# Kernel tuning notes

Measured on AMD Instinct MI355X. Metric: run time of the kernel, lower is better.

The kernel has to match this reference:

```python
import jax, jax.numpy as jnp
import numpy as np
from jax import lax


def _qconv_w(r, i, j, k):
    # Hamilton-product block kernel: components are (out/4, in/4, kh, kw) -> (out, in, kh, kw)
    row_r = jnp.concatenate([r, -i, -j, -k], axis=1)
    row_i = jnp.concatenate([i, r, -k, j], axis=1)
    row_j = jnp.concatenate([j, k, r, -i], axis=1)
    row_k = jnp.concatenate([k, -j, i, r], axis=1)
    return jnp.concatenate([row_r, row_i, row_j, row_k], axis=0)


def _conv3x3(x, W, b):
    y = lax.conv_general_dilated(x, W, window_strides=(1, 1), padding=((1, 1), (1, 1)),
                                 dimension_numbers=('NCHW', 'OIHW', 'NCHW'))
    return y + b[None, :, None, None]


def _qbn(x, gamma, beta, eps=1e-5):
    # Quaternion BN: global per-component mean, shared scalar quaternion variance
    r, i, j, k = jnp.split(x, 4, axis=1)
    dr, di, dj, dk = r - r.mean(), i - i.mean(), j - j.mean(), k - k.mean()
    var = (dr * dr + di * di + dj * dj + dk * dk).mean()
    inv = 1.0 / jnp.sqrt(var + eps)
    br, bi, bj, bk = jnp.split(beta, 4, axis=1)
    return jnp.concatenate([gamma * dr * inv + br, gamma * di * inv + bi,
                            gamma * dj * inv + bj, gamma * dk * inv + bk], axis=1)


def _pool2(x):
    b, c, h, w = x.shape
    return x.reshape(b, c, h // 2, 2, w // 2, 2).mean(axis=(3, 5))


def _qlin_w(r, i, j, k):
    # components (in/4, out/4) -> (in, out)
    col_r = jnp.concatenate([r, -i, -j, -k], axis=0)
    col_i = jnp.concatenate([i, r, -k, j], axis=0)
    col_j = jnp.concatenate([j, k, r, -i], axis=0)
    col_k = jnp.concatenate([k, -j, i, r], axis=0)
    return jnp.concatenate([col_r, col_i, col_j, col_k], axis=1)


def _forward(x, w_eca, l1_r, l1_i, l1_j, l1_k, l1_b, bn1_gamma, bn1_beta,
             l2_r, l2_i, l2_j, l2_k, l2_b, bn2_gamma, bn2_beta,
             l3_r, l3_i, l3_j, l3_k, l3_b, bn3_gamma, bn3_beta,
             fc_r, fc_i, fc_j, fc_k, fc_b):
    # ---- pre_press: eca_layer(k_size=1) top-3 channel selection + zero quaternion channel
    pooled = x.mean(axis=(2, 3))                      # [B, C] global avg pool
    att = jax.nn.softmax(w_eca[0] * pooled, axis=1)   # 1x1 conv1d == scalar scale, softmax over channels
    _, idx = lax.top_k(att, 3)                        # sorted descending, matches torch.topk
    top3 = jnp.take_along_axis(x, idx[:, :, None, None], axis=1)  # [B, 3, H, W]
    q = jnp.concatenate([jnp.zeros_like(top3[:, :1]), top3], axis=1)  # [B, 4, H, W]
    # ---- QConvEtAl: only layer1..3 are used in forward
    h = _conv3x3(q, _qconv_w(l1_r, l1_i, l1_j, l1_k), l1_b)
    h = _pool2(jax.nn.relu(_qbn(h, bn1_gamma, bn1_beta)))
    h = _conv3x3(h, _qconv_w(l2_r, l2_i, l2_j, l2_k), l2_b)
    h = _pool2(jax.nn.relu(_qbn(h, bn2_gamma, bn2_beta)))
    h = _conv3x3(h, _qconv_w(l3_r, l3_i, l3_j, l3_k), l3_b)
    h = _pool2(jax.nn.relu(_qbn(h, bn3_gamma, bn3_beta)))
    h = h.reshape(h.shape[0], -1)                     # [B, 128*(P/8)^2]
    return h @ _qlin_w(fc_r, fc_i, fc_j, fc_k) + fc_b


def setup_inputs() -> dict:
    key = jax.random.key(0)
    ks = jax.random.split(key, 20)
    rn = lambda k, s, sc=0.1: (jax.random.normal(k, s) * sc).astype(jnp.float32)
    inp = {
        'x': jax.random.normal(ks[0], (256, 200, 32, 32), dtype=jnp.float32),
        'w_eca': rn(ks[1], (1,), 1.0),
        'l1_r': rn(ks[2], (4, 1, 3, 3)), 'l1_i': rn(ks[3], (4, 1, 3, 3)),
        'l1_j': rn(ks[4], (4, 1, 3, 3)), 'l1_k': rn(ks[5], (4, 1, 3, 3)),
        'l1_b': jnp.zeros((16,), jnp.float32),
        'bn1_gamma': jnp.ones((1, 4, 1, 1), jnp.float32), 'bn1_beta': jnp.zeros((1, 16, 1, 1), jnp.float32),
        'l2_r': rn(ks[6], (16, 4, 3, 3)), 'l2_i': rn(ks[7], (16, 4, 3, 3)),
        'l2_j': rn(ks[8], (16, 4, 3, 3)), 'l2_k': rn(ks[9], (16, 4, 3, 3)),
        'l2_b': jnp.zeros((64,), jnp.float32),
        'bn2_gamma': jnp.ones((1, 16, 1, 1), jnp.float32), 'bn2_beta': jnp.zeros((1, 64, 1, 1), jnp.float32),
        'l3_r': rn(ks[10], (32, 16, 3, 3)), 'l3_i': rn(ks[11], (32, 16, 3, 3)),
        'l3_j': rn(ks[12], (32, 16, 3, 3)), 'l3_k': rn(ks[13], (32, 16, 3, 3)),
        'l3_b': jnp.zeros((128,), jnp.float32),
        'bn3_gamma': jnp.ones((1, 32, 1, 1), jnp.float32), 'bn3_beta': jnp.zeros((1, 128, 1, 1), jnp.float32),
        'fc_r': rn(ks[14], (512, 4)), 'fc_i': rn(ks[15], (512, 4)),
        'fc_j': rn(ks[16], (512, 4)), 'fc_k': rn(ks[17], (512, 4)),
        'fc_b': jnp.zeros((16,), jnp.float32),
    }
    return inp


def reference(x, w_eca, l1_r, l1_i, l1_j, l1_k, l1_b, bn1_gamma, bn1_beta,
              l2_r, l2_i, l2_j, l2_k, l2_b, bn2_gamma, bn2_beta,
              l3_r, l3_i, l3_j, l3_k, l3_b, bn3_gamma, bn3_beta,
              fc_r, fc_i, fc_j, fc_k, fc_b):
    return _forward(x, w_eca, l1_r, l1_i, l1_j, l1_k, l1_b, bn1_gamma, bn1_beta,
                    l2_r, l2_i, l2_j, l2_k, l2_b, bn2_gamma, bn2_beta,
                    l3_r, l3_i, l3_j, l3_k, l3_b, bn3_gamma, bn3_beta,
                    fc_r, fc_i, fc_j, fc_k, fc_b)
```

## Files before the change

### kernel.cpp

```cpp
#include <hip/hip_runtime.h>
#include <math.h>

#define WS_STATS 0
#define WS_W1    32
#define WS_W2    640
#define WS_W3    9856
#define WS_WFC   83584
#define WS_POOL  116352
#define WS_OUT1  167552
#define WS_OUT2  4361856
#define WS_OUT3  8556160

__device__ const int   d_TC[4][4] = {{0,1,2,3},{1,0,3,2},{2,3,0,1},{3,2,1,0}};
__device__ const float d_TS[4][4] = {{1.f,-1.f,-1.f,-1.f},{1.f,1.f,-1.f,1.f},
                                     {1.f,1.f,1.f,-1.f},{1.f,-1.f,1.f,1.f}};

__global__ __launch_bounds__(256) void prepmean_kernel(
    const float* __restrict__ x, float* __restrict__ pooled,
    const float* l1r, const float* l1i, const float* l1j, const float* l1k,
    const float* l2r, const float* l2i, const float* l2j, const float* l2k,
    const float* l3r, const float* l3i, const float* l3j, const float* l3k,
    const float* fcr, const float* fci, const float* fcj, const float* fck,
    float* ws)
{
    const int blk = blockIdx.x, t = threadIdx.x;
    const int lane = t & 63, wv = t >> 6;
    int tid = blk * 256 + t;
    const int nthr = 1024 * 256;
    if (tid < 24) ws[WS_STATS + tid] = 0.f;

    {
        const float* cp[4] = {l1r, l1i, l1j, l1k};
        for (int e = tid; e < 576; e += nthr) {
            int s = e / 144, rem = e % 144, k = rem / 16, oc = rem % 16;
            int p = oc >> 2, o = oc & 3;
            ws[WS_W1 + e] = d_TS[p][s] * cp[d_TC[p][s]][o * 9 + k];
        }
    }
    {
        const float* cp[4] = {l2r, l2i, l2j, l2k};
        for (int e = tid; e < 9216; e += nthr) {
            int oc = e & 63, k = (e >> 6) % 9, ic = e / 576;
            int p = oc >> 4, o = oc & 15, s = ic >> 2, ii = ic & 3;
            ws[WS_W2 + e] = d_TS[p][s] * cp[d_TC[p][s]][(o * 4 + ii) * 9 + k];
        }
    }
    {
        const float* cp[4] = {l3r, l3i, l3j, l3k};
        for (int e = tid; e < 73728; e += nthr) {
            int oc = e & 127, k = (e >> 7) % 9, ic = e / 1152;
            int p = oc >> 5, o = oc & 31, s = ic >> 4, ii = ic & 15;
            ws[WS_W3 + e] = d_TS[p][s] * cp[d_TC[p][s]][(o * 16 + ii) * 9 + k];
        }
    }
    {
        const float* cp[4] = {fcr, fci, fcj, fck};
        for (int e = tid; e < 32768; e += nthr) {
            int R = e >> 4, C = e & 15;
            int p = R >> 9, rr = R & 511, q = C >> 2, cc = C & 3;
            ws[WS_WFC + e] = d_TS[q][p] * cp[d_TC[q][p]][rr * 4 + cc];
        }
    }
    int base = blk * 50;
    for (int i = wv; i < 50; i += 4) {
        const float4* src = reinterpret_cast<const float4*>(x + (size_t)(base + i) * 1024);
        float s = 0.f;
        #pragma unroll
        for (int j = 0; j < 4; j++) {
            float4 v = src[lane + 64 * j];
            s += v.x + v.y + v.z + v.w;
        }
        #pragma unroll
        for (int off = 32; off; off >>= 1) s += __shfl_xor(s, off, 64);
        if (lane == 0) pooled[base + i] = s * (1.0f / 1024.0f);
    }
}

__global__ __launch_bounds__(256) void conv1_kernel(const float* __restrict__ x,
                                                    const float* __restrict__ pooled,
                                                    const float* __restrict__ w_eca,
                                                    const float* __restrict__ W1,
                                                    const float* __restrict__ b1,
                                                    float* __restrict__ out1,
                                                    float* __restrict__ stats)
{
    __shared__ float smem[3][6][36];
    __shared__ float rs[8];
    __shared__ int idx_s[3];
    int b = blockIdx.x >> 3, rg = blockIdx.x & 7;
    int t = threadIdx.x;
    if (t < 8) rs[t] = 0.f;
    if (t < 64) {
        float w = w_eca[0];
        float v[4]; int c[4];
        #pragma unroll
        for (int i = 0; i < 4; i++) {
            int ch = t + 64 * i;
            c[i] = ch;
            v[i] = (ch < 200) ? w * pooled[b * 200 + ch] : -INFINITY;
        }
        for (int k = 0; k < 3; k++) {
            float bv = -INFINITY; int bi = 0x3fffffff;
            #pragma unroll
            for (int i = 0; i < 4; i++)
                if (v[i] > bv || (v[i] == bv && c[i] < bi)) { bv = v[i]; bi = c[i]; }
            for (int off = 32; off; off >>= 1) {
                float ov = __shfl_xor(bv, off, 64);
                int   oi = __shfl_xor(bi, off, 64);
                if (ov > bv || (ov == bv && oi < bi)) { bv = ov; bi = oi; }
            }
            if (t == 0) idx_s[k] = bi;
            #pragma unroll
            for (int i = 0; i < 4; i++) if (c[i] == bi) v[i] = -INFINITY;
        }
    }
    __syncthreads();
    for (int i = t; i < 648; i += 256) {
        int s = i / 216, rem = i % 216, r = rem / 36, cc = rem % 36;
        int gr = rg * 4 - 1 + r, gc = cc - 1;
        float v = 0.f;
        if (gr >= 0 && gr < 32 && gc >= 0 && gc < 32)
            v = x[((size_t)b * 200 + idx_s[s]) * 1024 + gr * 32 + gc];
        smem[s][r][cc] = v;
    }
    __syncthreads();

    int oc = t & 15, rp = (t >> 4) & 3, ch = t >> 6;
    float bb = b1[oc];
    float acc[8];
    #pragma unroll
    for (int px = 0; px < 8; px++) acc[px] = bb;

    #pragma unroll
    for (int s = 0; s < 3; s++) {
        float w[9];
        #pragma unroll
        for (int k = 0; k < 9; k++) w[k] = W1[((s + 1) * 9 + k) * 16 + oc];
        float rowv[3][12];
        #pragma unroll
        for (int dy = 0; dy < 3; dy++) {
            const float* rb = &smem[s][rp + dy][ch * 8];
            float4 a = *reinterpret_cast<const float4*>(rb);
            float4 bq = *reinterpret_cast<const float4*>(rb + 4);
            float4 cq = *reinterpret_cast<const float4*>(rb + 8);
            rowv[dy][0]=a.x;  rowv[dy][1]=a.y;  rowv[dy][2]=a.z;  rowv[dy][3]=a.w;
            rowv[dy][4]=bq.x; rowv[dy][5]=bq.y; rowv[dy][6]=bq.z; rowv[dy][7]=bq.w;
            rowv[dy][8]=cq.x; rowv[dy][9]=cq.y; rowv[dy][10]=cq.z; rowv[dy][11]=cq.w;
        }
        #pragma unroll
        for (int dy = 0; dy < 3; dy++)
            #pragma unroll
            for (int px = 0; px < 8; px++) {
                float a = acc[px];
                a = fmaf(w[dy*3+0], rowv[dy][px],   a);
                a = fmaf(w[dy*3+1], rowv[dy][px+1], a);
                a = fmaf(w[dy*3+2], rowv[dy][px+2], a);
                acc[px] = a;
            }
    }
    int row = rg * 4 + rp;
    float* outb = out1 + ((size_t)b * 16 + oc) * 1024 + row * 32 + ch * 8;
    *reinterpret_cast<float4*>(outb)     = make_float4(acc[0], acc[1], acc[2], acc[3]);
    *reinterpret_cast<float4*>(outb + 4) = make_float4(acc[4], acc[5], acc[6], acc[7]);
    float sv = 0.f, qv = 0.f;
    #pragma unroll
    for (int px = 0; px < 8; px++) { sv += acc[px]; qv += acc[px] * acc[px]; }
    int g = oc >> 2;
    atomicAdd(&rs[g], sv); atomicAdd(&rs[4 + g], qv);
    __syncthreads();
    if (t < 8) atomicAdd(&stats[t], rs[t]);
}

__global__ __launch_bounds__(256) void conv2_kernel(const float* __restrict__ out1,
                                                    const float* __restrict__ W2,
                                                    const float* __restrict__ b2,
                                                    const float* __restrict__ bn1g,
                                                    const float* __restrict__ bn1b,
                                                    float* __restrict__ out2,
                                                    float* __restrict__ stats)
{
    __shared__ float smem[16][4][20];
    __shared__ float rs[8];
    __shared__ float sc[16], sh[16];
    int b = blockIdx.x >> 3, rq = blockIdx.x & 7;
    int t = threadIdx.x;
    if (t < 8) rs[t] = 0.f;
    if (t < 16) {
        const float invN = 1.0f / 1048576.0f;
        float var = 0.f;
        #pragma unroll
        for (int g = 0; g < 4; g++) {
            float S = stats[g], Q = stats[4 + g];
            var += Q - S * S * invN;
        }
        var *= invN;
        float inv = 1.0f / sqrtf(var + 1e-5f);
        float scale = bn1g[t & 3] * inv;
        sc[t] = scale;
        sh[t] = bn1b[t] - stats[t >> 2] * invN * scale;
    }
    __syncthreads();
    for (int i = t; i < 1280; i += 256) {
        int ic = i / 80, rem = i % 80, r = rem / 20, cc = rem % 20;
        int gr = rq * 2 - 1 + r, gc = cc - 1;
        float v = 0.f;
        if (gr >= 0 && gr < 16 && gc >= 0 && gc < 16) {
            const float* base = out1 + ((size_t)(b * 16 + ic) * 32 + 2 * gr) * 32 + 2 * gc;
            float2 a = *reinterpret_cast<const float2*>(base);
            float2 d = *reinterpret_cast<const float2*>(base + 32);
            float s0 = sc[ic], s1 = sh[ic];
            v = 0.25f * (fmaxf(fmaf(a.x, s0, s1), 0.f) + fmaxf(fmaf(a.y, s0, s1), 0.f)
                       + fmaxf(fmaf(d.x, s0, s1), 0.f) + fmaxf(fmaf(d.y, s0, s1), 0.f));
        }
        smem[ic][r][cc] = v;
    }
    __syncthreads();

    int oc = t & 63, rp = (t >> 6) & 1, ch = t >> 7;
    float bb = b2[oc];
    float acc[8];
    #pragma unroll
    for (int px = 0; px < 8; px++) acc[px] = bb;

    const float* Wp = W2 + oc;
    float w[9], wn[9];
    #pragma unroll
    for (int k = 0; k < 9; k++) w[k] = Wp[k * 64];
    for (int ic = 0; ic < 16; ic++) {
        if (ic < 15) {
            #pragma unroll
            for (int k = 0; k < 9; k++) wn[k] = Wp[(ic + 1) * 576 + k * 64];
        }
        float rowv[3][12];
        #pragma unroll
        for (int dy = 0; dy < 3; dy++) {
            const float* rb = &smem[ic][rp + dy][ch * 8];
            float4 a = *reinterpret_cast<const float4*>(rb);
            float4 bq = *reinterpret_cast<const float4*>(rb + 4);
            float4 cq = *reinterpret_cast<const float4*>(rb + 8);
            rowv[dy][0]=a.x;  rowv[dy][1]=a.y;  rowv[dy][2]=a.z;  rowv[dy][3]=a.w;
            rowv[dy][4]=bq.x; rowv[dy][5]=bq.y; rowv[dy][6]=bq.z; rowv[dy][7]=bq.w;
            rowv[dy][8]=cq.x; rowv[dy][9]=cq.y; rowv[dy][10]=cq.z; rowv[dy][11]=cq.w;
        }
        #pragma unroll
        for (int dy = 0; dy < 3; dy++)
            #pragma unroll
            for (int px = 0; px < 8; px++) {
                float a = acc[px];
                a = fmaf(w[dy*3+0], rowv[dy][px],   a);
                a = fmaf(w[dy*3+1], rowv[dy][px+1], a);
                a = fmaf(w[dy*3+2], rowv[dy][px+2], a);
                acc[px] = a;
            }
        if (ic < 15) {
            #pragma unroll
            for (int k = 0; k < 9; k++) w[k] = wn[k];
        }
    }
    int row = rq * 2 + rp;
    float* outb = out2 + ((size_t)b * 64 + oc) * 256 + row * 16 + ch * 8;
    *reinterpret_cast<float4*>(outb)     = make_float4(acc[0], acc[1], acc[2], acc[3]);
    *reinterpret_cast<float4*>(outb + 4) = make_float4(acc[4], acc[5], acc[6], acc[7]);
    float sv = 0.f, qv = 0.f;
    #pragma unroll
    for (int px = 0; px < 8; px++) { sv += acc[px]; qv += acc[px] * acc[px]; }
    int g = oc >> 4;
    atomicAdd(&rs[g], sv); atomicAdd(&rs[4 + g], qv);
    __syncthreads();
    if (t < 8) atomicAdd(&stats[8 + t], rs[t]);
}

__global__ __launch_bounds__(256) void conv3_kernel(const float* __restrict__ out2,
                                                    const float* __restrict__ W3,
                                                    const float* __restrict__ b3,
                                                    const float* __restrict__ bn2g,
                                                    const float* __restrict__ bn2b,
                                                    float* __restrict__ out3,
                                                    float* __restrict__ stats)
{
    __shared__ float smem[64][4][12];
    __shared__ float rs[8];
    __shared__ float sc[64], sh[64];
    int b = blockIdx.x >> 2, rh = blockIdx.x & 3;
    int t = threadIdx.x;
    if (t < 8) rs[t] = 0.f;
    if (t < 64) {
        const float invN = 1.0f / 1048576.0f;
        float var = 0.f;
        #pragma unroll
        for (int g = 0; g < 4; g++) {
            float S = stats[8 + g], Q = stats[12 + g];
            var += Q - S * S * invN;
        }
        var *= invN;
        float inv = 1.0f / sqrtf(var + 1e-5f);
        float scale = bn2g[t & 15] * inv;
        sc[t] = scale;
        sh[t] = bn2b[t] - stats[8 + (t >> 4)] * invN * scale;
    }
    __syncthreads();
    for (int i = t; i < 3072; i += 256) {
        int ic = i / 48, rem = i % 48, r = rem / 12, cc = rem % 12;
        int gr = rh * 2 - 1 + r, gc = cc - 1;
        float v = 0.f;
        if (gr >= 0 && gr < 8 && gc >= 0 && gc < 8) {
            const float* base = out2 + ((size_t)(b * 64 + ic) * 16 + 2 * gr) * 16 + 2 * gc;
            float2 a = *reinterpret_cast<const float2*>(base);
            float2 d = *reinterpret_cast<const float2*>(base + 16);
            float s0 = sc[ic], s1 = sh[ic];
            v = 0.25f * (fmaxf(fmaf(a.x, s0, s1), 0.f) + fmaxf(fmaf(a.y, s0, s1), 0.f)
                       + fmaxf(fmaf(d.x, s0, s1), 0.f) + fmaxf(fmaf(d.y, s0, s1), 0.f));
        }
        smem[ic][r][cc] = v;
    }
    __syncthreads();

    int oc = t & 127, rp = t >> 7;
    float bb = b3[oc];
    float acc[8];
    #pragma unroll
    for (int px = 0; px < 8; px++) acc[px] = bb;

    const float* Wp = W3 + oc;
    float w[9], wn[9];
    #pragma unroll
    for (int k = 0; k < 9; k++) w[k] = Wp[k * 128];
    for (int ic = 0; ic < 64; ic++) {
        if (ic < 63) {
            #pragma unroll
            for (int k = 0; k < 9; k++) wn[k] = Wp[(ic + 1) * 1152 + k * 128];
        }
        float rowv[3][12];
        #pragma unroll
        for (int dy = 0; dy < 3; dy++) {
            const float* rb = &smem[ic][rp + dy][0];
            float4 a = *reinterpret_cast<const float4*>(rb);
            float4 bq = *reinterpret_cast<const float4*>(rb + 4);
            float4 cq = *reinterpret_cast<const float4*>(rb + 8);
            rowv[dy][0]=a.x;  rowv[dy][1]=a.y;  rowv[dy][2]=a.z;  rowv[dy][3]=a.w;
            rowv[dy][4]=bq.x; rowv[dy][5]=bq.y; rowv[dy][6]=bq.z; rowv[dy][7]=bq.w;
            rowv[dy][8]=cq.x; rowv[dy][9]=cq.y; rowv[dy][10]=cq.z; rowv[dy][11]=cq.w;
        }
        #pragma unroll
        for (int dy = 0; dy < 3; dy++)
            #pragma unroll
            for (int px = 0; px < 8; px++) {
                float a = acc[px];
                a = fmaf(w[dy*3+0], rowv[dy][px],   a);
                a = fmaf(w[dy*3+1], rowv[dy][px+1], a);
                a = fmaf(w[dy*3+2], rowv[dy][px+2], a);
                acc[px] = a;
            }
        if (ic < 63) {
            #pragma unroll
            for (int k = 0; k < 9; k++) w[k] = wn[k];
        }
    }
    int row = rh * 2 + rp;
    float* outb = out3 + ((size_t)b * 128 + oc) * 64 + row * 8;
    *reinterpret_cast<float4*>(outb)     = make_float4(acc[0], acc[1], acc[2], acc[3]);
    *reinterpret_cast<float4*>(outb + 4) = make_float4(acc[4], acc[5], acc[6], acc[7]);
    float sv = 0.f, qv = 0.f;
    #pragma unroll
    for (int px = 0; px < 8; px++) { sv += acc[px]; qv += acc[px] * acc[px]; }
    int g = oc >> 5;
    atomicAdd(&rs[g], sv); atomicAdd(&rs[4 + g], qv);
    __syncthreads();
    if (t < 8) atomicAdd(&stats[16 + t], rs[t]);
}

__global__ __launch_bounds__(256) void fc_kernel(const float* __restrict__ out3,
                                                 const float* __restrict__ WFC,
                                                 const float* __restrict__ fcb,
                                                 const float* __restrict__ bn3g,
                                                 const float* __restrict__ bn3b,
                                                 const float* __restrict__ stats,
                                                 float* __restrict__ out)
{
    __shared__ float p3s[2048];
    __shared__ float sc[128], sh[128];
    __shared__ float red[256];
    int b = blockIdx.x, t = threadIdx.x;
    if (t < 128) {
        const float invN = 1.0f / 524288.0f;
        float var = 0.f;
        #pragma unroll
        for (int g = 0; g < 4; g++) {
            float S = stats[16 + g], Q = stats[20 + g];
            var += Q - S * S * invN;
        }
        var *= invN;
        float inv = 1.0f / sqrtf(var + 1e-5f);
        float scale = bn3g[t & 31] * inv;
        sc[t] = scale;
        sh[t] = bn3b[t] - stats[16 + (t >> 5)] * invN * scale;
    }
    __syncthreads();
    for (int i = t; i < 2048; i += 256) {
        int c = i >> 4, rem = i & 15, pr = rem >> 2, pc = rem & 3;
        const float* base = out3 + ((size_t)(b * 128 + c) * 8 + 2 * pr) * 8 + 2 * pc;
        float2 a = *reinterpret_cast<const float2*>(base);
        float2 d = *reinterpret_cast<const float2*>(base + 8);
        float s0 = sc[c], s1 = sh[c];
        p3s[i] = 0.25f * (fmaxf(fmaf(a.x, s0, s1), 0.f) + fmaxf(fmaf(a.y, s0, s1), 0.f)
                        + fmaxf(fmaf(d.x, s0, s1), 0.f) + fmaxf(fmaf(d.y, s0, s1), 0.f));
    }
    __syncthreads();
    int col = t & 15, fr = t >> 4;
    float s = 0.f;
    for (int i = 0; i < 128; i++) {
        int f = i * 16 + fr;
        s = fmaf(p3s[f], WFC[f * 16 + col], s);
    }
    red[t] = s;
    __syncthreads();
    for (int st = 128; st >= 16; st >>= 1) {
        if (t < st) red[t] += red[t + st];
        __syncthreads();
    }
    if (t < 16) out[b * 16 + t] = red[t] + fcb[t];
}

extern "C" void kernel_launch(void* const* d_in, const int* in_sizes, int n_in,
                              void* d_out, int out_size, void* d_ws, size_t ws_size,
                              hipStream_t stream)
{
    (void)in_sizes; (void)n_in; (void)out_size; (void)ws_size;
    const float* x     = (const float*)d_in[0];
    const float* w_eca = (const float*)d_in[1];
    const float* l1r = (const float*)d_in[2],  *l1i = (const float*)d_in[3];
    const float* l1j = (const float*)d_in[4],  *l1k = (const float*)d_in[5];
    const float* l1b = (const float*)d_in[6];
    const float* bn1g = (const float*)d_in[7], *bn1b = (const float*)d_in[8];
    const float* l2r = (const float*)d_in[9],  *l2i = (const float*)d_in[10];
    const float* l2j = (const float*)d_in[11], *l2k = (const float*)d_in[12];
    const float* l2b = (const float*)d_in[13];
    const float* bn2g = (const float*)d_in[14], *bn2b = (const float*)d_in[15];
    const float* l3r = (const float*)d_in[16], *l3i = (const float*)d_in[17];
    const float* l3j = (const float*)d_in[18], *l3k = (const float*)d_in[19];
    const float* l3b = (const float*)d_in[20];
    const float* bn3g = (const float*)d_in[21], *bn3b = (const float*)d_in[22];
    const float* fcr = (const float*)d_in[23], *fci = (const float*)d_in[24];
    const float* fcj = (const float*)d_in[25], *fck = (const float*)d_in[26];
    const float* fcb = (const float*)d_in[27];

    float* ws   = (float*)d_ws;
    float* outp = (float*)d_out;

    prepmean_kernel<<<1024, 256, 0, stream>>>(x, ws + WS_POOL,
        l1r, l1i, l1j, l1k, l2r, l2i, l2j, l2k, l3r, l3i, l3j, l3k,
        fcr, fci, fcj, fck, ws);
    conv1_kernel<<<2048, 256, 0, stream>>>(x, ws + WS_POOL, w_eca, ws + WS_W1,
                                           l1b, ws + WS_OUT1, ws + WS_STATS);
    conv2_kernel<<<2048, 256, 0, stream>>>(ws + WS_OUT1, ws + WS_W2, l2b, bn1g, bn1b,
                                           ws + WS_OUT2, ws + WS_STATS);
    conv3_kernel<<<1024, 256, 0, stream>>>(ws + WS_OUT2, ws + WS_W3, l3b, bn2g, bn2b,
                                           ws + WS_OUT3, ws + WS_STATS);
    fc_kernel<<<256, 256, 0, stream>>>(ws + WS_OUT3, ws + WS_WFC, fcb, bn3g, bn3b,
                                       ws + WS_STATS, outp);
}
```

Before: 185.0 us.

## Fuse all stages into one cooperative persistent kernel with grid syncs

Replaces the five separate kernel launches with a single cooperative kernel of 1024 blocks that runs weight prep, pooling, the three conv stages and the FC stage, separated by grid.sync barriers. Grids larger than 1024 blocks are handled by looping over the work. The goal is to remove per-launch overhead and the gaps between launches. The cost is grid-wide barrier latency, occupancy limited by the union of shared memory, and a fallback to the old multi-kernel path if the cooperative launch fails.

```diff
diff --git a/kernel.cpp b/kernel.cpp
--- a/kernel.cpp
+++ b/kernel.cpp
@@ -1,5 +1,8 @@
 #include <hip/hip_runtime.h>
+#include <hip/hip_cooperative_groups.h>
 #include <math.h>
+
+namespace cg = cooperative_groups;
 
 #define WS_STATS 0
 #define WS_W1    32
@@ -15,22 +18,25 @@
 __device__ const float d_TS[4][4] = {{1.f,-1.f,-1.f,-1.f},{1.f,1.f,-1.f,1.f},
                                      {1.f,1.f,1.f,-1.f},{1.f,-1.f,1.f,1.f}};
 
-__global__ __launch_bounds__(256) void prepmean_kernel(
-    const float* __restrict__ x, float* __restrict__ pooled,
-    const float* l1r, const float* l1i, const float* l1j, const float* l1k,
-    const float* l2r, const float* l2i, const float* l2j, const float* l2k,
-    const float* l3r, const float* l3i, const float* l3j, const float* l3k,
-    const float* fcr, const float* fci, const float* fcj, const float* fck,
-    float* ws)
-{
-    const int blk = blockIdx.x, t = threadIdx.x;
-    const int lane = t & 63, wv = t >> 6;
-    int tid = blk * 256 + t;
-    const int nthr = 1024 * 256;
+struct Params {
+    const float *x, *w_eca;
+    const float *l1b, *bn1g, *bn1b;
+    const float *l2b, *bn2g, *bn2b;
+    const float *l3b, *bn3g, *bn3b;
+    const float *fcb;
+    const float *l1r, *l1i, *l1j, *l1k;
+    const float *l2r, *l2i, *l2j, *l2k;
+    const float *l3r, *l3i, *l3j, *l3k;
+    const float *fcr, *fci, *fcj, *fck;
+    float *ws, *out;
+};
+
+__device__ __forceinline__ void prep_weights(const Params& P, int tid, int nthr)
+{
+    float* ws = P.ws;
     if (tid < 24) ws[WS_STATS + tid] = 0.f;
-
     {
-        const float* cp[4] = {l1r, l1i, l1j, l1k};
+        const float* cp[4] = {P.l1r, P.l1i, P.l1j, P.l1k};
         for (int e = tid; e < 576; e += nthr) {
             int s = e / 144, rem = e % 144, k = rem / 16, oc = rem % 16;
             int p = oc >> 2, o = oc & 3;
@@ -38,7 +44,7 @@
         }
     }
     {
-        const float* cp[4] = {l2r, l2i, l2j, l2k};
+        const float* cp[4] = {P.l2r, P.l2i, P.l2j, P.l2k};
         for (int e = tid; e < 9216; e += nthr) {
             int oc = e & 63, k = (e >> 6) % 9, ic = e / 576;
             int p = oc >> 4, o = oc & 15, s = ic >> 2, ii = ic & 3;
@@ -46,7 +52,7 @@
         }
     }
     {
-        const float* cp[4] = {l3r, l3i, l3j, l3k};
+        const float* cp[4] = {P.l3r, P.l3i, P.l3j, P.l3k};
         for (int e = tid; e < 73728; e += nthr) {
             int oc = e & 127, k = (e >> 7) % 9, ic = e / 1152;
             int p = oc >> 5, o = oc & 31, s = ic >> 4, ii = ic & 15;
@@ -54,13 +60,19 @@
         }
     }
     {
-        const float* cp[4] = {fcr, fci, fcj, fck};
+        const float* cp[4] = {P.fcr, P.fci, P.fcj, P.fck};
         for (int e = tid; e < 32768; e += nthr) {
             int R = e >> 4, C = e & 15;
             int p = R >> 9, rr = R & 511, q = C >> 2, cc = C & 3;
             ws[WS_WFC + e] = d_TS[q][p] * cp[d_TC[q][p]][rr * 4 + cc];
         }
     }
+}
+
+__device__ __forceinline__ void mean_channels(const float* __restrict__ x,
+                                              float* __restrict__ pooled,
+                                              int blk, int wv, int lane)
+{
     int base = blk * 50;
     for (int i = wv; i < 50; i += 4) {
         const float4* src = reinterpret_cast<const float4*>(x + (size_t)(base + i) * 1024);
@@ -76,57 +88,64 @@
     }
 }
 
-__global__ __launch_bounds__(256) void conv1_kernel(const float* __restrict__ x,
-                                                    const float* __restrict__ pooled,
-                                                    const float* __restrict__ w_eca,
-                                                    const float* __restrict__ W1,
-                                                    const float* __restrict__ b1,
-                                                    float* __restrict__ out1,
-                                                    float* __restrict__ stats)
+__device__ __forceinline__ void top3(const float* __restrict__ pooled, float w,
+                                     int b, int lane, int& idx0, int& idx1, int& idx2)
+{
+    float v[4]; int c[4];
+    #pragma unroll
+    for (int i = 0; i < 4; i++) {
+        int ch = lane + 64 * i;
+        c[i] = ch;
+        v[i] = (ch < 200) ? w * pooled[b * 200 + ch] : -INFINITY;
+    }
+    idx0 = idx1 = idx2 = 0;
+    for (int k = 0; k < 3; k++) {
+        float bv = -INFINITY; int bi = 0x3fffffff;
+        #pragma unroll
+        for (int i = 0; i < 4; i++)
+            if (v[i] > bv || (v[i] == bv && c[i] < bi)) { bv = v[i]; bi = c[i]; }
+        for (int off = 32; off; off >>= 1) {
+            float ov = __shfl_xor(bv, off, 64);
+            int   oi = __shfl_xor(bi, off, 64);
+            if (ov > bv || (ov == bv && oi < bi)) { bv = ov; bi = oi; }
+        }
+        if (k == 0) idx0 = bi; else if (k == 1) idx1 = bi; else idx2 = bi;
+        #pragma unroll
+        for (int i = 0; i < 4; i++) if (c[i] == bi) v[i] = -INFINITY;
+    }
+}
+
+__global__ __launch_bounds__(256) void prepmean_kernel(Params P)
+{
+    const int blk = blockIdx.x, t = threadIdx.x;
+    prep_weights(P, blk * 256 + t, 1024 * 256);
+    mean_channels(P.x, P.ws + WS_POOL, blk, t >> 6, t & 63);
+}
+
+__global__ __launch_bounds__(256) void conv1_kernel(Params P)
 {
     __shared__ float smem[3][6][36];
     __shared__ float rs[8];
-    __shared__ int idx_s[3];
+    float* ws = P.ws;
+    const float* pooled = ws + WS_POOL;
     int b = blockIdx.x >> 3, rg = blockIdx.x & 7;
-    int t = threadIdx.x;
+    int t = threadIdx.x, lane = t & 63;
     if (t < 8) rs[t] = 0.f;
-    if (t < 64) {
-        float w = w_eca[0];
-        float v[4]; int c[4];
-        #pragma unroll
-        for (int i = 0; i < 4; i++) {
-            int ch = t + 64 * i;
-            c[i] = ch;
-            v[i] = (ch < 200) ? w * pooled[b * 200 + ch] : -INFINITY;
-        }
-        for (int k = 0; k < 3; k++) {
-            float bv = -INFINITY; int bi = 0x3fffffff;
-            #pragma unroll
-            for (int i = 0; i < 4; i++)
-                if (v[i] > bv || (v[i] == bv && c[i] < bi)) { bv = v[i]; bi = c[i]; }
-            for (int off = 32; off; off >>= 1) {
-                float ov = __shfl_xor(bv, off, 64);
-                int   oi = __shfl_xor(bi, off, 64);
-                if (ov > bv || (ov == bv && oi < bi)) { bv = ov; bi = oi; }
-            }
-            if (t == 0) idx_s[k] = bi;
-            #pragma unroll
-            for (int i = 0; i < 4; i++) if (c[i] == bi) v[i] = -INFINITY;
-        }
-    }
-    __syncthreads();
+    int idx0, idx1, idx2;
+    top3(pooled, P.w_eca[0], b, lane, idx0, idx1, idx2);
     for (int i = t; i < 648; i += 256) {
         int s = i / 216, rem = i % 216, r = rem / 36, cc = rem % 36;
         int gr = rg * 4 - 1 + r, gc = cc - 1;
+        int idx = (s == 0) ? idx0 : (s == 1 ? idx1 : idx2);
         float v = 0.f;
         if (gr >= 0 && gr < 32 && gc >= 0 && gc < 32)
-            v = x[((size_t)b * 200 + idx_s[s]) * 1024 + gr * 32 + gc];
+            v = P.x[((size_t)b * 200 + idx) * 1024 + gr * 32 + gc];
         smem[s][r][cc] = v;
     }
     __syncthreads();
 
     int oc = t & 15, rp = (t >> 4) & 3, ch = t >> 6;
-    float bb = b1[oc];
+    float bb = P.l1b[oc];
     float acc[8];
     #pragma unroll
     for (int px = 0; px < 8; px++) acc[px] = bb;
@@ -135,7 +154,7 @@
     for (int s = 0; s < 3; s++) {
         float w[9];
         #pragma unroll
-        for (int k = 0; k < 9; k++) w[k] = W1[((s + 1) * 9 + k) * 16 + oc];
+        for (int k = 0; k < 9; k++) w[k] = ws[WS_W1 + ((s + 1) * 9 + k) * 16 + oc];
         float rowv[3][12];
         #pragma unroll
         for (int dy = 0; dy < 3; dy++) {
@@ -159,7 +178,7 @@
             }
     }
     int row = rg * 4 + rp;
-    float* outb = out1 + ((size_t)b * 16 + oc) * 1024 + row * 32 + ch * 8;
+    float* outb = ws + WS_OUT1 + ((size_t)b * 16 + oc) * 1024 + row * 32 + ch * 8;
     *reinterpret_cast<float4*>(outb)     = make_float4(acc[0], acc[1], acc[2], acc[3]);
     *reinterpret_cast<float4*>(outb + 4) = make_float4(acc[4], acc[5], acc[6], acc[7]);
     float sv = 0.f, qv = 0.f;
@@ -168,20 +187,15 @@
     int g = oc >> 2;
     atomicAdd(&rs[g], sv); atomicAdd(&rs[4 + g], qv);
     __syncthreads();
-    if (t < 8) atomicAdd(&stats[t], rs[t]);
-}
-
-__global__ __launch_bounds__(256) void conv2_kernel(const float* __restrict__ out1,
-                                                    const float* __restrict__ W2,
-                                                    const float* __restrict__ b2,
-                                                    const float* __restrict__ bn1g,
-                                                    const float* __restrict__ bn1b,
-                                                    float* __restrict__ out2,
-                                                    float* __restrict__ stats)
+    if (t < 8) atomicAdd(&ws[WS_STATS + t], rs[t]);
+}
+
+__global__ __launch_bounds__(256) void conv2_kernel(Params P)
 {
     __shared__ float smem[16][4][20];
     __shared__ float rs[8];
     __shared__ float sc[16], sh[16];
+    float* ws = P.ws;
     int b = blockIdx.x >> 3, rq = blockIdx.x & 7;
     int t = threadIdx.x;
     if (t < 8) rs[t] = 0.f;
@@ -190,14 +204,14 @@
         float var = 0.f;
         #pragma unroll
         for (int g = 0; g < 4; g++) {
-            float S = stats[g], Q = stats[4 + g];
+            float S = ws[WS_STATS + g], Q = ws[WS_STATS + 4 + g];
             var += Q - S * S * invN;
         }
         var *= invN;
         float inv = 1.0f / sqrtf(var + 1e-5f);
-        float scale = bn1g[t & 3] * inv;
+        float scale = P.bn1g[t & 3] * inv;
         sc[t] = scale;
-        sh[t] = bn1b[t] - stats[t >> 2] * invN * scale;
+        sh[t] = P.bn1b[t] - ws[WS_STATS + (t >> 2)] * invN * scale;
     }
     __syncthreads();
     for (int i = t; i < 1280; i += 256) {
@@ -205,7 +219,7 @@
         int gr = rq * 2 - 1 + r, gc = cc - 1;
         float v = 0.f;
         if (gr >= 0 && gr < 16 && gc >= 0 && gc < 16) {
-            const float* base = out1 + ((size_t)(b * 16 + ic) * 32 + 2 * gr) * 32 + 2 * gc;
+            const float* base = ws + WS_OUT1 + ((size_t)(b * 16 + ic) * 32 + 2 * gr) * 32 + 2 * gc;
             float2 a = *reinterpret_cast<const float2*>(base);
             float2 d = *reinterpret_cast<const float2*>(base + 32);
             float s0 = sc[ic], s1 = sh[ic];
@@ -217,12 +231,12 @@
     __syncthreads();
 
     int oc = t & 63, rp = (t >> 6) & 1, ch = t >> 7;
-    float bb = b2[oc];
+    float bb = P.l2b[oc];
     float acc[8];
     #pragma unroll
     for (int px = 0; px < 8; px++) acc[px] = bb;
 
-    const float* Wp = W2 + oc;
+    const float* Wp = ws + WS_W2 + oc;
     float w[9], wn[9];
     #pragma unroll
     for (int k = 0; k < 9; k++) w[k] = Wp[k * 64];
@@ -258,7 +272,7 @@
         }
     }
     int row = rq * 2 + rp;
-    float* outb = out2 + ((size_t)b * 64 + oc) * 256 + row * 16 + ch * 8;
+    float* outb = ws + WS_OUT2 + ((size_t)b * 64 + oc) * 256 + row * 16 + ch * 8;
     *reinterpret_cast<float4*>(outb)     = make_float4(acc[0], acc[1], acc[2], acc[3]);
     *reinterpret_cast<float4*>(outb + 4) = make_float4(acc[4], acc[5], acc[6], acc[7]);
     float sv = 0.f, qv = 0.f;
@@ -267,20 +281,15 @@
     int g = oc >> 4;
     atomicAdd(&rs[g], sv); atomicAdd(&rs[4 + g], qv);
     __syncthreads();
-    if (t < 8) atomicAdd(&stats[8 + t], rs[t]);
-}
-
-__global__ __launch_bounds__(256) void conv3_kernel(const float* __restrict__ out2,
-                                                    const float* __restrict__ W3,
-                                                    const float* __restrict__ b3,
-                                                    const float* __restrict__ bn2g,
-                                                    const float* __restrict__ bn2b,
-                                                    float* __restrict__ out3,
-                                                    float* __restrict__ stats)
+    if (t < 8) atomicAdd(&ws[WS_STATS + 8 + t], rs[t]);
+}
+
+__global__ __launch_bounds__(256) void conv3_kernel(Params P)
 {
     __shared__ float smem[64][4][12];
     __shared__ float rs[8];
     __shared__ float sc[64], sh[64];
+    float* ws = P.ws;
     int b = blockIdx.x >> 2, rh = blockIdx.x & 3;
     int t = threadIdx.x;
     if (t < 8) rs[t] = 0.f;
@@ -289,14 +298,14 @@
         float var = 0.f;
         #pragma unroll
         for (int g = 0; g < 4; g++) {
-            float S = stats[8 + g], Q = stats[12 + g];
+            float S = ws[WS_STATS + 8 + g], Q = ws[WS_STATS + 12 + g];
             var += Q - S * S * invN;
         }
         var *= invN;
         float inv = 1.0f / sqrtf(var + 1e-5f);
-        float scale = bn2g[t & 15] * inv;
+        float scale = P.bn2g[t & 15] * inv;
         sc[t] = scale;
-        sh[t] = bn2b[t] - stats[8 + (t >> 4)] * invN * scale;
+        sh[t] = P.bn2b[t] - ws[WS_STATS + 8 + (t >> 4)] * invN * scale;
     }
     __syncthreads();
     for (int i = t; i < 3072; i += 256) {
@@ -304,7 +313,7 @@
         int gr = rh * 2 - 1 + r, gc = cc - 1;
         float v = 0.f;
         if (gr >= 0 && gr < 8 && gc >= 0 && gc < 8) {
-            const float* base = out2 + ((size_t)(b * 64 + ic) * 16 + 2 * gr) * 16 + 2 * gc;
+            const float* base = ws + WS_OUT2 + ((size_t)(b * 64 + ic) * 16 + 2 * gr) * 16 + 2 * gc;
             float2 a = *reinterpret_cast<const float2*>(base);
             float2 d = *reinterpret_cast<const float2*>(base + 16);
             float s0 = sc[ic], s1 = sh[ic];
@@ -316,12 +325,12 @@
     __syncthreads();
 
     int oc = t & 127, rp = t >> 7;
-    float bb = b3[oc];
+    float bb = P.l3b[oc];
     float acc[8];
     #pragma unroll
     for (int px = 0; px < 8; px++) acc[px] = bb;
 
-    const float* Wp = W3 + oc;
+    const float* Wp = ws + WS_W3 + oc;
     float w[9], wn[9];
     #pragma unroll
     for (int k = 0; k < 9; k++) w[k] = Wp[k * 128];
@@ -357,7 +366,7 @@
         }
     }
     int row = rh * 2 + rp;
-    float* outb = out3 + ((size_t)b * 128 + oc) * 64 + row * 8;
+    float* outb = ws + WS_OUT3 + ((size_t)b * 128 + oc) * 64 + row * 8;
     *reinterpret_cast<float4*>(outb)     = make_float4(acc[0], acc[1], acc[2], acc[3]);
     *reinterpret_cast<float4*>(outb + 4) = make_float4(acc[4], acc[5], acc[6], acc[7]);
     float sv = 0.f, qv = 0.f;
@@ -366,39 +375,34 @@
     int g = oc >> 5;
     atomicAdd(&rs[g], sv); atomicAdd(&rs[4 + g], qv);
     __syncthreads();
-    if (t < 8) atomicAdd(&stats[16 + t], rs[t]);
-}
-
-__global__ __launch_bounds__(256) void fc_kernel(const float* __restrict__ out3,
-                                                 const float* __restrict__ WFC,
-                                                 const float* __restrict__ fcb,
-                                                 const float* __restrict__ bn3g,
-                                                 const float* __restrict__ bn3b,
-                                                 const float* __restrict__ stats,
-                                                 float* __restrict__ out)
+    if (t < 8) atomicAdd(&ws[WS_STATS + 16 + t], rs[t]);
+}
+
+__global__ __launch_bounds__(256) void fc_kernel(Params P)
 {
     __shared__ float p3s[2048];
     __shared__ float sc[128], sh[128];
     __shared__ float red[256];
+    float* ws = P.ws;
     int b = blockIdx.x, t = threadIdx.x;
     if (t < 128) {
         const float invN = 1.0f / 524288.0f;
         float var = 0.f;
         #pragma unroll
         for (int g = 0; g < 4; g++) {
-            float S = stats[16 + g], Q = stats[20 + g];
+            float S = ws[WS_STATS + 16 + g], Q = ws[WS_STATS + 20 + g];
             var += Q - S * S * invN;
         }
         var *= invN;
         float inv = 1.0f / sqrtf(var + 1e-5f);
-        float scale = bn3g[t & 31] * inv;
+        float scale = P.bn3g[t & 31] * inv;
         sc[t] = scale;
-        sh[t] = bn3b[t] - stats[16 + (t >> 5)] * invN * scale;
+        sh[t] = P.bn3b[t] - ws[WS_STATS + 16 + (t >> 5)] * invN * scale;
     }
     __syncthreads();
     for (int i = t; i < 2048; i += 256) {
         int c = i >> 4, rem = i & 15, pr = rem >> 2, pc = rem & 3;
-        const float* base = out3 + ((size_t)(b * 128 + c) * 8 + 2 * pr) * 8 + 2 * pc;
+        const float* base = ws + WS_OUT3 + ((size_t)(b * 128 + c) * 8 + 2 * pr) * 8 + 2 * pc;
         float2 a = *reinterpret_cast<const float2*>(base);
         float2 d = *reinterpret_cast<const float2*>(base + 8);
         float s0 = sc[c], s1 = sh[c];
@@ -410,7 +414,7 @@
     float s = 0.f;
     for (int i = 0; i < 128; i++) {
         int f = i * 16 + fr;
-        s = fmaf(p3s[f], WFC[f * 16 + col], s);
+        s = fmaf(p3s[f], ws[WS_WFC + f * 16 + col], s);
     }
     red[t] = s;
     __syncthreads();
@@ -418,7 +422,314 @@
         if (t < st) red[t] += red[t + st];
         __syncthreads();
     }
-    if (t < 16) out[b * 16 + t] = red[t] + fcb[t];
+    if (t < 16) P.out[b * 16 + t] = red[t] + P.fcb[t];
+}
+
+__global__ __launch_bounds__(256, 4) void qcnet_kernel(Params P)
+{
+    cg::grid_group grid = cg::this_grid();
+    __shared__ union {
+        struct { float smem[3][6][36];  float rs[8]; } c1;
+        struct { float smem[16][4][20]; float sc[16];  float sh[16];  float rs[8]; } c2;
+        struct { float smem[64][4][12]; float sc[64];  float sh[64];  float rs[8]; } c3;
+        struct { float p3s[2048]; float red[256]; float sc[128]; float sh[128]; } fcu;
+    } U;
+
+    const int blk = blockIdx.x, t = threadIdx.x;
+    const int lane = t & 63, wv = t >> 6;
+    float* ws = P.ws;
+
+    prep_weights(P, blk * 256 + t, 1024 * 256);
+    mean_channels(P.x, ws + WS_POOL, blk, wv, lane);
+    grid.sync();
+
+    {
+        int b = blk >> 2;
+        int idx0, idx1, idx2;
+        top3(ws + WS_POOL, P.w_eca[0], b, lane, idx0, idx1, idx2);
+        for (int u = 0; u < 2; u++) {
+            int rg = ((blk & 3) << 1) | u;
+            if (t < 8) U.c1.rs[t] = 0.f;
+            for (int i = t; i < 648; i += 256) {
+                int s = i / 216, rem = i % 216, r = rem / 36, cc = rem % 36;
+                int gr = rg * 4 - 1 + r, gc = cc - 1;
+                int idx = (s == 0) ? idx0 : (s == 1 ? idx1 : idx2);
+                float vv = 0.f;
+                if (gr >= 0 && gr < 32 && gc >= 0 && gc < 32)
+                    vv = P.x[((size_t)b * 200 + idx) * 1024 + gr * 32 + gc];
+                U.c1.smem[s][r][cc] = vv;
+            }
+            __syncthreads();
+
+            int oc = t & 15, rp = (t >> 4) & 3, ch = t >> 6;
+            float bb = P.l1b[oc];
+            float acc[8];
+            #pragma unroll
+            for (int px = 0; px < 8; px++) acc[px] = bb;
+
+            #pragma unroll
+            for (int s = 0; s < 3; s++) {
+                float wk[9];
+                #pragma unroll
+                for (int k = 0; k < 9; k++) wk[k] = ws[WS_W1 + ((s + 1) * 9 + k) * 16 + oc];
+                float rowv[3][12];
+                #pragma unroll
+                for (int dy = 0; dy < 3; dy++) {
+                    const float* rb = &U.c1.smem[s][rp + dy][ch * 8];
+                    float4 a = *reinterpret_cast<const float4*>(rb);
+                    float4 bq = *reinterpret_cast<const float4*>(rb + 4);
+                    float4 cq = *reinterpret_cast<const float4*>(rb + 8);
+                    rowv[dy][0]=a.x;  rowv[dy][1]=a.y;  rowv[dy][2]=a.z;  rowv[dy][3]=a.w;
+                    rowv[dy][4]=bq.x; rowv[dy][5]=bq.y; rowv[dy][6]=bq.z; rowv[dy][7]=bq.w;
+                    rowv[dy][8]=cq.x; rowv[dy][9]=cq.y; rowv[dy][10]=cq.z; rowv[dy][11]=cq.w;
+                }
+                #pragma unroll
+                for (int dy = 0; dy < 3; dy++)
+                    #pragma unroll
+                    for (int px = 0; px < 8; px++) {
+                        float a = acc[px];
+                        a = fmaf(wk[dy*3+0], rowv[dy][px],   a);
+                        a = fmaf(wk[dy*3+1], rowv[dy][px+1], a);
+                        a = fmaf(wk[dy*3+2], rowv[dy][px+2], a);
+                        acc[px] = a;
+                    }
+            }
+            int row = rg * 4 + rp;
+            float* outb = ws + WS_OUT1 + ((size_t)b * 16 + oc) * 1024 + row * 32 + ch * 8;
+            *reinterpret_cast<float4*>(outb)     = make_float4(acc[0], acc[1], acc[2], acc[3]);
+            *reinterpret_cast<float4*>(outb + 4) = make_float4(acc[4], acc[5], acc[6], acc[7]);
+            float sv = 0.f, qv = 0.f;
+            #pragma unroll
+            for (int px = 0; px < 8; px++) { sv += acc[px]; qv += acc[px] * acc[px]; }
+            atomicAdd(&U.c1.rs[oc >> 2], sv); atomicAdd(&U.c1.rs[4 + (oc >> 2)], qv);
+            __syncthreads();
+            if (t < 8) atomicAdd(&ws[WS_STATS + t], U.c1.rs[t]);
+            __syncthreads();
+        }
+    }
+    grid.sync();
+
+    {
+        for (int u = 0; u < 2; u++) {
+            int unit = blk * 2 + u;
+            int b = unit >> 3, rq = unit & 7;
+            if (t < 8) U.c2.rs[t] = 0.f;
+            if (t < 16) {
+                const float invN = 1.0f / 1048576.0f;
+                float var = 0.f;
+                #pragma unroll
+                for (int g = 0; g < 4; g++) {
+                    float S = ws[WS_STATS + g], Q = ws[WS_STATS + 4 + g];
+                    var += Q - S * S * invN;
+                }
+                var *= invN;
+                float inv = 1.0f / sqrtf(var + 1e-5f);
+                float scale = P.bn1g[t & 3] * inv;
+                U.c2.sc[t] = scale;
+                U.c2.sh[t] = P.bn1b[t] - ws[WS_STATS + (t >> 2)] * invN * scale;
+            }
+            __syncthreads();
+            for (int i = t; i < 1280; i += 256) {
+                int ic = i / 80, rem = i % 80, r = rem / 20, cc = rem % 20;
+                int gr = rq * 2 - 1 + r, gc = cc - 1;
+                float vv = 0.f;
+                if (gr >= 0 && gr < 16 && gc >= 0 && gc < 16) {
+                    const float* base = ws + WS_OUT1 + ((size_t)(b * 16 + ic) * 32 + 2 * gr) * 32 + 2 * gc;
+                    float2 a = *reinterpret_cast<const float2*>(base);
+                    float2 d = *reinterpret_cast<const float2*>(base + 32);
+                    float s0 = U.c2.sc[ic], s1 = U.c2.sh[ic];
+                    vv = 0.25f * (fmaxf(fmaf(a.x, s0, s1), 0.f) + fmaxf(fmaf(a.y, s0, s1), 0.f)
+                                + fmaxf(fmaf(d.x, s0, s1), 0.f) + fmaxf(fmaf(d.y, s0, s1), 0.f));
+                }
+                U.c2.smem[ic][r][cc] = vv;
+            }
+            __syncthreads();
+
+            int oc = t & 63, rp = (t >> 6) & 1, ch = t >> 7;
+            float bb = P.l2b[oc];
+            float acc[8];
+            #pragma unroll
+            for (int px = 0; px < 8; px++) acc[px] = bb;
+
+            const float* Wp = ws + WS_W2 + oc;
+            float wk[9], wn[9];
+            #pragma unroll
+            for (int k = 0; k < 9; k++) wk[k] = Wp[k * 64];
+            for (int ic = 0; ic < 16; ic++) {
+                if (ic < 15) {
+                    #pragma unroll
+                    for (int k = 0; k < 9; k++) wn[k] = Wp[(ic + 1) * 576 + k * 64];
+                }
+                float rowv[3][12];
+                #pragma unroll
+                for (int dy = 0; dy < 3; dy++) {
+                    const float* rb = &U.c2.smem[ic][rp + dy][ch * 8];
+                    float4 a = *reinterpret_cast<const float4*>(rb);
+                    float4 bq = *reinterpret_cast<const float4*>(rb + 4);
+                    float4 cq = *reinterpret_cast<const float4*>(rb + 8);
+                    rowv[dy][0]=a.x;  rowv[dy][1]=a.y;  rowv[dy][2]=a.z;  rowv[dy][3]=a.w;
+                    rowv[dy][4]=bq.x; rowv[dy][5]=bq.y; rowv[dy][6]=bq.z; rowv[dy][7]=bq.w;
+                    rowv[dy][8]=cq.x; rowv[dy][9]=cq.y; rowv[dy][10]=cq.z; rowv[dy][11]=cq.w;
+                }
+                #pragma unroll
+                for (int dy = 0; dy < 3; dy++)
+                    #pragma unroll
+                    for (int px = 0; px < 8; px++) {
+                        float a = acc[px];
+                        a = fmaf(wk[dy*3+0], rowv[dy][px],   a);
+                        a = fmaf(wk[dy*3+1], rowv[dy][px+1], a);
+                        a = fmaf(wk[dy*3+2], rowv[dy][px+2], a);
+                        acc[px] = a;
+                    }
+                if (ic < 15) {
+                    #pragma unroll
+                    for (int k = 0; k < 9; k++) wk[k] = wn[k];
+                }
+            }
+            int row = rq * 2 + rp;
+            float* outb = ws + WS_OUT2 + ((size_t)b * 64 + oc) * 256 + row * 16 + ch * 8;
+            *reinterpret_cast<float4*>(outb)     = make_float4(acc[0], acc[1], acc[2], acc[3]);
+            *reinterpret_cast<float4*>(outb + 4) = make_float4(acc[4], acc[5], acc[6], acc[7]);
+            float sv = 0.f, qv = 0.f;
+            #pragma unroll
+            for (int px = 0; px < 8; px++) { sv += acc[px]; qv += acc[px] * acc[px]; }
+            atomicAdd(&U.c2.rs[oc >> 4], sv); atomicAdd(&U.c2.rs[4 + (oc >> 4)], qv);
+            __syncthreads();
+            if (t < 8) atomicAdd(&ws[WS_STATS + 8 + t], U.c2.rs[t]);
+            __syncthreads();
+        }
+    }
+    grid.sync();
+
+    {
+        int b = blk >> 2, rh = blk & 3;
+        if (t < 8) U.c3.rs[t] = 0.f;
+        if (t < 64) {
+            const float invN = 1.0f / 1048576.0f;
+            float var = 0.f;
+            #pragma unroll
+            for (int g = 0; g < 4; g++) {
+                float S = ws[WS_STATS + 8 + g], Q = ws[WS_STATS + 12 + g];
+                var += Q - S * S * invN;
+            }
+            var *= invN;
+            float inv = 1.0f / sqrtf(var + 1e-5f);
+            float scale = P.bn2g[t & 15] * inv;
+            U.c3.sc[t] = scale;
+            U.c3.sh[t] = P.bn2b[t] - ws[WS_STATS + 8 + (t >> 4)] * invN * scale;
+        }
+        __syncthreads();
+        for (int i = t; i < 3072; i += 256) {
+            int ic = i / 48, rem = i % 48, r = rem / 12, cc = rem % 12;
+            int gr = rh * 2 - 1 + r, gc = cc - 1;
+            float vv = 0.f;
+            if (gr >= 0 && gr < 8 && gc >= 0 && gc < 8) {
+                const float* base = ws + WS_OUT2 + ((size_t)(b * 64 + ic) * 16 + 2 * gr) * 16 + 2 * gc;
+                float2 a = *reinterpret_cast<const float2*>(base);
+                float2 d = *reinterpret_cast<const float2*>(base + 16);
+                float s0 = U.c3.sc[ic], s1 = U.c3.sh[ic];
+                vv = 0.25f * (fmaxf(fmaf(a.x, s0, s1), 0.f) + fmaxf(fmaf(a.y, s0, s1), 0.f)
+                            + fmaxf(fmaf(d.x, s0, s1), 0.f) + fmaxf(fmaf(d.y, s0, s1), 0.f));
+            }
+            U.c3.smem[ic][r][cc] = vv;
+        }
+        __syncthreads();
+
+        int oc = t & 127, rp = t >> 7;
+        float bb = P.l3b[oc];
+        float acc[8];
+        #pragma unroll
+        for (int px = 0; px < 8; px++) acc[px] = bb;
+
+        const float* Wp = ws + WS_W3 + oc;
+        float wk[9], wn[9];
+        #pragma unroll
+        for (int k = 0; k < 9; k++) wk[k] = Wp[k * 128];
+        for (int ic = 0; ic < 64; ic++) {
+            if (ic < 63) {
+                #pragma unroll
+                for (int k = 0; k < 9; k++) wn[k] = Wp[(ic + 1) * 1152 + k * 128];
+            }
+            float rowv[3][12];
+            #pragma unroll
+            for (int dy = 0; dy < 3; dy++) {
+                const float* rb = &U.c3.smem[ic][rp + dy][0];
+                float4 a = *reinterpret_cast<const float4*>(rb);
+                float4 bq = *reinterpret_cast<const float4*>(rb + 4);
+                float4 cq = *reinterpret_cast<const float4*>(rb + 8);
+                rowv[dy][0]=a.x;  rowv[dy][1]=a.y;  rowv[dy][2]=a.z;  rowv[dy][3]=a.w;
+                rowv[dy][4]=bq.x; rowv[dy][5]=bq.y; rowv[dy][6]=bq.z; rowv[dy][7]=bq.w;
+                rowv[dy][8]=cq.x; rowv[dy][9]=cq.y; rowv[dy][10]=cq.z; rowv[dy][11]=cq.w;
+            }
+            #pragma unroll
+            for (int dy = 0; dy < 3; dy++)
+                #pragma unroll
+                for (int px = 0; px < 8; px++) {
+                    float a = acc[px];
+                    a = fmaf(wk[dy*3+0], rowv[dy][px],   a);
+                    a = fmaf(wk[dy*3+1], rowv[dy][px+1], a);
+                    a = fmaf(wk[dy*3+2], rowv[dy][px+2], a);
+                    acc[px] = a;
+                }
+            if (ic < 63) {
+                #pragma unroll
+                for (int k = 0; k < 9; k++) wk[k] = wn[k];
+            }
+        }
+        int row = rh * 2 + rp;
+        float* outb = ws + WS_OUT3 + ((size_t)b * 128 + oc) * 64 + row * 8;
+        *reinterpret_cast<float4*>(outb)     = make_float4(acc[0], acc[1], acc[2], acc[3]);
+        *reinterpret_cast<float4*>(outb + 4) = make_float4(acc[4], acc[5], acc[6], acc[7]);
+        float sv = 0.f, qv = 0.f;
+        #pragma unroll
+        for (int px = 0; px < 8; px++) { sv += acc[px]; qv += acc[px] * acc[px]; }
+        atomicAdd(&U.c3.rs[oc >> 5], sv); atomicAdd(&U.c3.rs[4 + (oc >> 5)], qv);
+        __syncthreads();
+        if (t < 8) atomicAdd(&ws[WS_STATS + 16 + t], U.c3.rs[t]);
+    }
+    grid.sync();
+
+    if (blk < 256) {
+        int b = blk;
+        if (t < 128) {
+            const float invN = 1.0f / 524288.0f;
+            float var = 0.f;
+            #pragma unroll
+            for (int g = 0; g < 4; g++) {
+                float S = ws[WS_STATS + 16 + g], Q = ws[WS_STATS + 20 + g];
+                var += Q - S * S * invN;
+            }
+            var *= invN;
+            float inv = 1.0f / sqrtf(var + 1e-5f);
+            float scale = P.bn3g[t & 31] * inv;
+            U.fcu.sc[t] = scale;
+            U.fcu.sh[t] = P.bn3b[t] - ws[WS_STATS + 16 + (t >> 5)] * invN * scale;
+        }
+        __syncthreads();
+        for (int i = t; i < 2048; i += 256) {
+            int c = i >> 4, rem = i & 15, pr = rem >> 2, pc = rem & 3;
+            const float* base = ws + WS_OUT3 + ((size_t)(b * 128 + c) * 8 + 2 * pr) * 8 + 2 * pc;
+            float2 a = *reinterpret_cast<const float2*>(base);
+            float2 d = *reinterpret_cast<const float2*>(base + 8);
+            float s0 = U.fcu.sc[c], s1 = U.fcu.sh[c];
+            U.fcu.p3s[i] = 0.25f * (fmaxf(fmaf(a.x, s0, s1), 0.f) + fmaxf(fmaf(a.y, s0, s1), 0.f)
+                                  + fmaxf(fmaf(d.x, s0, s1), 0.f) + fmaxf(fmaf(d.y, s0, s1), 0.f));
+        }
+        __syncthreads();
+        int col = t & 15, fr = t >> 4;
+        float s = 0.f;
+        for (int i = 0; i < 128; i++) {
+            int f = i * 16 + fr;
+            s = fmaf(U.fcu.p3s[f], ws[WS_WFC + f * 16 + col], s);
+        }
+        U.fcu.red[t] = s;
+        __syncthreads();
+        for (int st = 128; st >= 16; st >>= 1) {
+            if (t < st) U.fcu.red[t] += U.fcu.red[t + st];
+            __syncthreads();
+        }
+        if (t < 16) P.out[b * 16 + t] = U.fcu.red[t] + P.fcb[t];
+    }
 }
 
 extern "C" void kernel_launch(void* const* d_in, const int* in_sizes, int n_in,
@@ -426,36 +737,37 @@
                               hipStream_t stream)
 {
     (void)in_sizes; (void)n_in; (void)out_size; (void)ws_size;
-    const float* x     = (const float*)d_in[0];
-    const float* w_eca = (const float*)d_in[1];
-    const float* l1r = (const float*)d_in[2],  *l1i = (const float*)d_in[3];
-    const float* l1j = (const float*)d_in[4],  *l1k = (const float*)d_in[5];
-    const float* l1b = (const float*)d_in[6];
-    const float* bn1g = (const float*)d_in[7], *bn1b = (const float*)d_in[8];
-    const float* l2r = (const float*)d_in[9],  *l2i = (const float*)d_in[10];
-    const float* l2j = (const float*)d_in[11], *l2k = (const float*)d_in[12];
-    const float* l2b = (const float*)d_in[13];
-    const float* bn2g = (const float*)d_in[14], *bn2b = (const float*)d_in[15];
-    const float* l3r = (const float*)d_in[16], *l3i = (const float*)d_in[17];
-    const float* l3j = (const float*)d_in[18], *l3k = (const float*)d_in[19];
-    const float* l3b = (const float*)d_in[20];
-    const float* bn3g = (const float*)d_in[21], *bn3b = (const float*)d_in[22];
-    const float* fcr = (const float*)d_in[23], *fci = (const float*)d_in[24];
-    const float* fcj = (const float*)d_in[25], *fck = (const float*)d_in[26];
-    const float* fcb = (const float*)d_in[27];
-
-    float* ws   = (float*)d_ws;
-    float* outp = (float*)d_out;
-
-    prepmean_kernel<<<1024, 256, 0, stream>>>(x, ws + WS_POOL,
-        l1r, l1i, l1j, l1k, l2r, l2i, l2j, l2k, l3r, l3i, l3j, l3k,
-        fcr, fci, fcj, fck, ws);
-    conv1_kernel<<<2048, 256, 0, stream>>>(x, ws + WS_POOL, w_eca, ws + WS_W1,
-                                           l1b, ws + WS_OUT1, ws + WS_STATS);
-    conv2_kernel<<<2048, 256, 0, stream>>>(ws + WS_OUT1, ws + WS_W2, l2b, bn1g, bn1b,
-                                           ws + WS_OUT2, ws + WS_STATS);
-    conv3_kernel<<<1024, 256, 0, stream>>>(ws + WS_OUT2, ws + WS_W3, l3b, bn2g, bn2b,
-                                           ws + WS_OUT3, ws + WS_STATS);
-    fc_kernel<<<256, 256, 0, stream>>>(ws + WS_OUT3, ws + WS_WFC, fcb, bn3g, bn3b,
-                                       ws + WS_STATS, outp);
-}
+    Params P;
+    P.x    = (const float*)d_in[0];
+    P.w_eca= (const float*)d_in[1];
+    P.l1r  = (const float*)d_in[2];  P.l1i = (const float*)d_in[3];
+    P.l1j  = (const float*)d_in[4];  P.l1k = (const float*)d_in[5];
+    P.l1b  = (const float*)d_in[6];
+    P.bn1g = (const float*)d_in[7];  P.bn1b = (const float*)d_in[8];
+    P.l2r  = (const float*)d_in[9];  P.l2i = (const float*)d_in[10];
+    P.l2j  = (const float*)d_in[11]; P.l2k = (const float*)d_in[12];
+    P.l2b  = (const float*)d_in[13];
+    P.bn2g = (const float*)d_in[14]; P.bn2b = (const float*)d_in[15];
+    P.l3r  = (const float*)d_in[16]; P.l3i = (const float*)d_in[17];
+    P.l3j  = (const float*)d_in[18]; P.l3k = (const float*)d_in[19];
+    P.l3b  = (const float*)d_in[20];
+    P.bn3g = (const float*)d_in[21]; P.bn3b = (const float*)d_in[22];
+    P.fcr  = (const float*)d_in[23]; P.fci = (const float*)d_in[24];
+    P.fcj  = (const float*)d_in[25]; P.fck = (const float*)d_in[26];
+    P.fcb  = (const float*)d_in[27];
+    P.ws   = (float*)d_ws;
+    P.out  = (float*)d_out;
+
+    void* args[] = { (void*)&P };
+    hipError_t err = hipLaunchCooperativeKernel((const void*)qcnet_kernel,
+                                                dim3(1024), dim3(256),
+                                                args, 0, stream);
+    if (err != hipSuccess) {
+        (void)hipGetLastError();
+        prepmean_kernel<<<1024, 256, 0, stream>>>(P);
+        conv1_kernel<<<2048, 256, 0, stream>>>(P);
+        conv2_kernel<<<2048, 256, 0, stream>>>(P);
+        conv3_kernel<<<1024, 256, 0, stream>>>(P);
+        fc_kernel<<<256, 256, 0, stream>>>(P);
+    }
+}
```

Result: slower. 719.0 us (+288.7%).
